# Optimization experiments

Measured on AMD Instinct MI355X. Metric: run time of the kernel, lower is better.

Reference implementation:

```python
import jax, jax.numpy as jnp
import numpy as np

HEADS = 8  # from init_kwargs

def setup_inputs() -> dict:
    key = jax.random.key(0)
    ks = jax.random.split(key, 9)
    N, S, E = 8, 2048, 512
    scale = 1.0 / np.sqrt(E)
    return {
        "values": jax.random.normal(ks[0], (N, S, E), jnp.float32),
        "keys": jax.random.normal(ks[1], (N, S, E), jnp.float32),
        "query": jax.random.normal(ks[2], (N, S, E), jnp.float32),
        "mask": jnp.ones((N, 1, 1, S), jnp.int32),
        "Wv": jax.random.normal(ks[3], (E, E), jnp.float32) * scale,
        "Wk": jax.random.normal(ks[4], (E, E), jnp.float32) * scale,
        "Wq": jax.random.normal(ks[5], (E, E), jnp.float32) * scale,
        "Wo": jax.random.normal(ks[6], (E, E), jnp.float32) * scale,
        "bo": jnp.zeros((E,), jnp.float32),
    }

def reference(values, keys, query, mask, Wv, Wk, Wq, Wo, bo):
    N, Q, E = query.shape
    H = HEADS
    D = E // H
    v = (values @ Wv).reshape(N, -1, H, D)  # [N,K,H,D]
    k = (keys @ Wk).reshape(N, -1, H, D)
    q = (query @ Wq).reshape(N, Q, H, D)
    energy = jnp.einsum('nqhd,nkhd->nhqk', q, k)  # [N,H,Q,K]
    energy = jnp.where(mask == 0, jnp.float32(-1e20), energy)
    attn = jax.nn.softmax(energy / jnp.sqrt(jnp.float32(D)), axis=3)
    out = jnp.einsum('nhqk,nkhd->nqhd', attn, v).reshape(N, Q, E)
    return out @ Wo + bo
```

## Files before the change

### kernel.cpp

```cpp
#include <hip/hip_runtime.h>
#include <hip/hip_bf16.h>
#include <stdint.h>

typedef __bf16 bf16;
typedef __bf16 bf16x8 __attribute__((ext_vector_type(8)));
typedef __bf16 bf16x4v __attribute__((ext_vector_type(4)));
typedef float  f32x4  __attribute__((ext_vector_type(4)));
typedef float  f32x16 __attribute__((ext_vector_type(16)));
typedef unsigned int u32x4 __attribute__((ext_vector_type(4)));

#define NB    8
#define SEQ   2048
#define EMB   512
#define NHEAD 8
#define HD    64

static __device__ __forceinline__ f32x4 mfma16(bf16x8 a, bf16x8 b, f32x4 c) {
    return __builtin_amdgcn_mfma_f32_16x16x32_bf16(a, b, c, 0, 0, 0);
}
static __device__ __forceinline__ f32x16 mfma32(bf16x8 a, bf16x8 b, f32x16 c) {
    return __builtin_amdgcn_mfma_f32_32x32x16_bf16(a, b, c, 0, 0, 0);
}
static __device__ __forceinline__ float ex2(float x) {
    float r; asm("v_exp_f32 %0, %1" : "=v"(r) : "v"(x)); return r;
}
static __device__ __forceinline__ unsigned pkbf(float lo, float hi) {
    unsigned d; asm("v_cvt_pk_bf16_f32 %0, %1, %2" : "=v"(d) : "v"(lo), "v"(hi)); return d;
}
static __device__ __forceinline__ void gload_lds16(const void* g, void* l) {
    __builtin_amdgcn_global_load_lds(
        (const __attribute__((address_space(1))) unsigned int*)g,
        (__attribute__((address_space(3))) unsigned int*)l, 16, 0, 0);
}

__global__ __launch_bounds__(256) void prep_weights(
    const float* __restrict__ Wv, const float* __restrict__ Wk,
    const float* __restrict__ Wq, const float* __restrict__ Wo,
    bf16* __restrict__ wt)
{
    int idx = blockIdx.x * 256 + threadIdx.x;
    int w   = idx >> 18;
    int rem = idx & 262143;
    int k   = rem >> 9;
    int n   = rem & 511;
    const float* src = (w == 0) ? Wv : (w == 1) ? Wk : (w == 2) ? Wq : Wo;
    wt[(size_t)w * 262144 + (size_t)n * 512 + k] = (bf16)src[k * 512 + n];
}

template <bool A_F32, bool FINAL>
__global__ __launch_bounds__(256) void gemm_kernel(
    const void* __restrict__ Ap, const bf16* __restrict__ Bt,
    void* __restrict__ Cp, const float* __restrict__ bias)
{
    __shared__ __align__(16) bf16 As[128][72];
    __shared__ __align__(16) bf16 Bs[128][72];

    const int t    = threadIdx.x;
    const int lane = t & 63;
    const int wave = t >> 6;
    const int wr   = wave >> 1, wc = wave & 1;
    const int l15  = lane & 15, lg = lane >> 4;
    const long row0 = (long)blockIdx.x * 128;
    const int  col0 = blockIdx.y * 128;

    f32x4 acc[4][4];
#pragma unroll
    for (int i = 0; i < 4; i++)
#pragma unroll
        for (int j = 0; j < 4; j++) acc[i][j] = (f32x4){0.f, 0.f, 0.f, 0.f};

    for (int k0 = 0; k0 < 512; k0 += 64) {
        __syncthreads();
        if (A_F32) {
            const float* A = (const float*)Ap;
#pragma unroll
            for (int i = 0; i < 8; i++) {
                int c  = t + 256 * i;
                int r  = c >> 4;
                int cc = (c & 15) * 4;
                f32x4 v = *(const f32x4*)(A + (row0 + r) * 512 + k0 + cc);
                bf16x4v pk = { (bf16)v[0], (bf16)v[1], (bf16)v[2], (bf16)v[3] };
                *(bf16x4v*)&As[r][cc] = pk;
            }
        } else {
            const bf16* A = (const bf16*)Ap;
#pragma unroll
            for (int i = 0; i < 4; i++) {
                int c  = t + 256 * i;
                int r  = c >> 3;
                int cc = (c & 7) * 8;
                *(bf16x8*)&As[r][cc] = *(const bf16x8*)(A + (row0 + r) * 512 + k0 + cc);
            }
        }
#pragma unroll
        for (int i = 0; i < 4; i++) {
            int c  = t + 256 * i;
            int r  = c >> 3;
            int cc = (c & 7) * 8;
            *(bf16x8*)&Bs[r][cc] = *(const bf16x8*)(Bt + (size_t)(col0 + r) * 512 + k0 + cc);
        }
        __syncthreads();
#pragma unroll
        for (int kc = 0; kc < 64; kc += 32) {
            bf16x8 af[4], bfv[4];
#pragma unroll
            for (int mb = 0; mb < 4; mb++)
                af[mb] = *(bf16x8*)&As[wr * 64 + mb * 16 + l15][kc + lg * 8];
#pragma unroll
            for (int nb = 0; nb < 4; nb++)
                bfv[nb] = *(bf16x8*)&Bs[wc * 64 + nb * 16 + l15][kc + lg * 8];
#pragma unroll
            for (int mb = 0; mb < 4; mb++)
#pragma unroll
                for (int nb = 0; nb < 4; nb++)
                    acc[mb][nb] = mfma16(af[mb], bfv[nb], acc[mb][nb]);
        }
    }

#pragma unroll
    for (int mb = 0; mb < 4; mb++)
#pragma unroll
        for (int nb = 0; nb < 4; nb++)
#pragma unroll
            for (int r = 0; r < 4; r++) {
                long grow = row0 + wr * 64 + mb * 16 + lg * 4 + r;
                int  gcol = col0 + wc * 64 + nb * 16 + l15;
                float v = acc[mb][nb][r];
                if (FINAL) {
                    ((float*)Cp)[grow * 512 + gcol] = v + bias[gcol];
                } else {
                    ((bf16*)Cp)[grow * 512 + gcol] = (bf16)v;
                }
            }
}

__global__ __launch_bounds__(512, 2) void attn_kernel(
    const bf16* __restrict__ Qg, const bf16* __restrict__ Kg,
    const bf16* __restrict__ Vg, const int* __restrict__ mask,
    bf16* __restrict__ ctx)
{
    __shared__ __align__(16) bf16 Ks[2][4096];
    __shared__ __align__(16) bf16 Vt[2][4096];
    __shared__ __align__(16) bf16 Ob[8][32 * 72];

    const int t    = threadIdx.x;
    const int lane = t & 63;
    const int w    = t >> 6;
    const int l31  = lane & 31;
    const int hi   = lane >> 5;
    const int qt = blockIdx.x, h = blockIdx.y, n = blockIdx.z;

    const size_t nbase   = (size_t)n * SEQ;
    const size_t headoff = (size_t)h * 64;
    const int q0 = qt * 512 + w * 64;

    bf16x8 qf[2][4];
#pragma unroll
    for (int qb = 0; qb < 2; ++qb)
#pragma unroll
        for (int ds = 0; ds < 4; ++ds)
            qf[qb][ds] = *(const bf16x8*)(Qg + (nbase + q0 + qb * 32 + l31) * 512 + headoff + ds * 16 + hi * 8);

    f32x16 o[2][2] = {};
    float m_run[2] = {-1e30f, -1e30f};
    float l_run[2] = {0.f, 0.f};

    const bf16* kg = Kg + (nbase + w * 8 + (lane >> 3)) * 512 + headoff + (((lane & 7) ^ (lane >> 3)) << 3);
    const bf16* vg = Vg + (nbase + lane) * 512 + headoff + w * 8;
    const int*  mp = mask + n * SEQ;

    gload_lds16(kg, (char*)&Ks[0][0] + w * 1024);
    {
        bf16x8 v0 = *(const bf16x8*)vg;
        char* vb = (char*)&Vt[0][0];
#pragma unroll
        for (int j = 0; j < 8; ++j)
            *(bf16*)(vb + (8 * w + j) * 128 + ((2 * lane) ^ (j << 4))) = v0[j];
    }
    __syncthreads();

    const float SC = 0.18033688011f;

    int cur = 0;
    for (int kt = 0; kt < 32; ++kt) {
        bf16x8 vstage;
        if (kt < 31) {
            gload_lds16(kg + (size_t)(kt + 1) * 64 * 512, (char*)&Ks[cur ^ 1][0] + w * 1024);
            vstage = *(const bf16x8*)(vg + (size_t)(kt + 1) * 64 * 512);
        }
        int mv = mp[kt * 64 + lane];

        f32x16 p[2][2] = {};
        const char* kb_base = (const char*)&Ks[cur][0];
#pragma unroll
        for (int ds = 0; ds < 4; ++ds) {
            int sw = (ds * 32 + hi * 16) ^ ((l31 & 7) << 4);
            bf16x8 kf0 = *(const bf16x8*)(kb_base + (l31) * 128 + sw);
            bf16x8 kf1 = *(const bf16x8*)(kb_base + (32 + l31) * 128 + sw);
            p[0][0] = mfma32(kf0, qf[0][ds], p[0][0]);
            p[1][0] = mfma32(kf0, qf[1][ds], p[1][0]);
            p[0][1] = mfma32(kf1, qf[0][ds], p[0][1]);
            p[1][1] = mfma32(kf1, qf[1][ds], p[1][1]);
        }

        unsigned long long mb = __ballot(mv != 0);
        if (mb != ~0ULL) {
#pragma unroll
            for (int qb = 0; qb < 2; ++qb)
#pragma unroll
                for (int kb = 0; kb < 2; ++kb) {
                    float* pp = (float*)&p[qb][kb];
#pragma unroll
                    for (int r = 0; r < 16; ++r) {
                        int kk = kb * 32 + (r & 3) + 8 * (r >> 2) + 4 * hi;
                        if (!((mb >> kk) & 1)) pp[r] = -1e30f;
                    }
                }
        }

        u32x4 bq[2][4];
#pragma unroll
        for (int qb = 0; qb < 2; ++qb) {
            float* p0 = (float*)&p[qb][0];
            float* p1 = (float*)&p[qb][1];
            float tm = fmaxf(p0[0], p1[0]);
#pragma unroll
            for (int r = 1; r < 16; ++r) tm = fmaxf(tm, fmaxf(p0[r], p1[r]));
            float tms = tm * SC;
            float rmax = fmaxf(tms, __shfl_xor(tms, 32));
            if (!__all(rmax <= m_run[qb] + 8.0f)) {
                float mn  = fmaxf(m_run[qb], rmax);
                float fac = ex2(m_run[qb] - mn);
#pragma unroll
                for (int db = 0; db < 2; ++db) {
                    float* oo = (float*)&o[db][qb];
#pragma unroll
                    for (int r = 0; r < 16; ++r) oo[r] *= fac;
                }
                l_run[qb] *= fac;
                m_run[qb] = mn;
            }
            float negm = -m_run[qb];
            float sl = 0.f;
#pragma unroll
            for (int r = 0; r < 16; ++r) { float e = ex2(fmaf(p0[r], SC, negm)); p0[r] = e; sl += e; }
#pragma unroll
            for (int r = 0; r < 16; ++r) { float e = ex2(fmaf(p1[r], SC, negm)); p1[r] = e; sl += e; }
            l_run[qb] += sl + __shfl_xor(sl, 32);

#pragma unroll
            for (int ks = 0; ks < 4; ++ks) {
                float* ps = (ks >> 1) ? p1 : p0;
                int bo = (ks & 1) * 8;
                unsigned A  = pkbf(ps[bo + 0], ps[bo + 1]);
                unsigned B  = pkbf(ps[bo + 2], ps[bo + 3]);
                unsigned C  = pkbf(ps[bo + 4], ps[bo + 5]);
                unsigned Dw = pkbf(ps[bo + 6], ps[bo + 7]);
                unsigned xA = __shfl_xor(A, 32);
                unsigned xB = __shfl_xor(B, 32);
                unsigned xC = __shfl_xor(C, 32);
                unsigned xD = __shfl_xor(Dw, 32);
                unsigned w0 = hi ? xC : A;
                unsigned w1 = hi ? xD : B;
                unsigned w2 = hi ? C : xA;
                unsigned w3 = hi ? Dw : xB;
                bq[qb][ks] = (u32x4){w0, w1, w2, w3};
            }
        }

        const char* vb_base = (const char*)&Vt[cur][0];
#pragma unroll
        for (int ks = 0; ks < 4; ++ks) {
            int sw = (ks * 32 + hi * 16) ^ ((l31 & 7) << 4);
            bf16x8 vf0 = *(const bf16x8*)(vb_base + (l31) * 128 + sw);
            bf16x8 vf1 = *(const bf16x8*)(vb_base + (32 + l31) * 128 + sw);
            union { u32x4 u; bf16x8 v; } c0, c1;
            c0.u = bq[0][ks]; c1.u = bq[1][ks];
            o[0][0] = mfma32(vf0, c0.v, o[0][0]);
            o[0][1] = mfma32(vf0, c1.v, o[0][1]);
            o[1][0] = mfma32(vf1, c0.v, o[1][0]);
            o[1][1] = mfma32(vf1, c1.v, o[1][1]);
        }

        if (kt < 31) {
            char* vb = (char*)&Vt[cur ^ 1][0];
#pragma unroll
            for (int j = 0; j < 8; ++j)
                *(bf16*)(vb + (8 * w + j) * 128 + ((2 * lane) ^ (j << 4))) = vstage[j];
        }
        __syncthreads();
        cur ^= 1;
    }

#pragma unroll
    for (int qb = 0; qb < 2; ++qb) {
        float inv = 1.f / l_run[qb];
        bf16* ob = &Ob[w][0];
#pragma unroll
        for (int db = 0; db < 2; ++db) {
            float* oo = (float*)&o[db][qb];
#pragma unroll
            for (int r = 0; r < 16; ++r) {
                int d = db * 32 + (r & 3) + 8 * (r >> 2) + 4 * hi;
                ob[l31 * 72 + d] = (bf16)(oo[r] * inv);
            }
        }
#pragma unroll
        for (int i = 0; i < 2; ++i)
#pragma unroll
            for (int half = 0; half < 2; ++half) {
                int ql = i * 16 + (lane >> 2);
                int d8 = (lane & 3) * 8 + half * 32;
                bf16x8 vv = *(const bf16x8*)(ob + ql * 72 + d8);
                *(bf16x8*)(ctx + (nbase + q0 + qb * 32 + ql) * 512 + headoff + d8) = vv;
            }
    }
}

extern "C" void kernel_launch(void* const* d_in, const int* in_sizes, int n_in,
                              void* d_out, int out_size, void* d_ws, size_t ws_size,
                              hipStream_t stream) {
    (void)in_sizes; (void)n_in; (void)out_size; (void)ws_size;
    const float* values = (const float*)d_in[0];
    const float* keys   = (const float*)d_in[1];
    const float* query  = (const float*)d_in[2];
    const int*   mask   = (const int*)d_in[3];
    const float* Wv = (const float*)d_in[4];
    const float* Wk = (const float*)d_in[5];
    const float* Wq = (const float*)d_in[6];
    const float* Wo = (const float*)d_in[7];
    const float* bo = (const float*)d_in[8];
    float* out = (float*)d_out;

    char* ws = (char*)d_ws;
    bf16* wt = (bf16*)(ws);
    bf16* Qb = (bf16*)(ws + ((size_t)2  << 20));
    bf16* Kb = (bf16*)(ws + ((size_t)18 << 20));
    bf16* Vb = (bf16*)(ws + ((size_t)34 << 20));
    bf16* Cb = (bf16*)(ws + ((size_t)50 << 20));

    prep_weights<<<4096, 256, 0, stream>>>(Wv, Wk, Wq, Wo, wt);
    gemm_kernel<true, false><<<dim3(128, 4), 256, 0, stream>>>(values, wt,              Vb, nullptr);
    gemm_kernel<true, false><<<dim3(128, 4), 256, 0, stream>>>(keys,   wt + 262144,     Kb, nullptr);
    gemm_kernel<true, false><<<dim3(128, 4), 256, 0, stream>>>(query,  wt + 2 * 262144, Qb, nullptr);
    attn_kernel<<<dim3(4, 8, 8), 512, 0, stream>>>(Qb, Kb, Vb, mask, Cb);
    gemm_kernel<false, true><<<dim3(128, 4), 256, 0, stream>>>(Cb, wt + 3 * 262144, out, bo);
}
```

Measured before the change: 183.6 us.

## Halve attention query tile per wave to double grid and occupancy

Each wave in the attention kernel now handles 32 query rows instead of 64, so a block covers 256 queries. The grid grows from 256 to 512 blocks and launch bounds allow 4 blocks per CU. The aim is better CU fill and latency hiding on a 256-CU part. In exchange, each K/V tile loaded into LDS is reused across half as many queries, so K/V global traffic and LDS loads per FLOP double.

Measured after the change: 205.1 us. 11.7% more time.

```diff
diff --git a/kernel.cpp b/kernel.cpp
--- a/kernel.cpp
+++ b/kernel.cpp
@@ -134,7 +134,7 @@
             }
 }
 
-__global__ __launch_bounds__(512, 2) void attn_kernel(
+__global__ __launch_bounds__(512, 4) void attn_kernel(
     const bf16* __restrict__ Qg, const bf16* __restrict__ Kg,
     const bf16* __restrict__ Vg, const int* __restrict__ mask,
     bf16* __restrict__ ctx)
@@ -152,18 +152,16 @@
 
     const size_t nbase   = (size_t)n * SEQ;
     const size_t headoff = (size_t)h * 64;
-    const int q0 = qt * 512 + w * 64;
-
-    bf16x8 qf[2][4];
-#pragma unroll
-    for (int qb = 0; qb < 2; ++qb)
-#pragma unroll
-        for (int ds = 0; ds < 4; ++ds)
-            qf[qb][ds] = *(const bf16x8*)(Qg + (nbase + q0 + qb * 32 + l31) * 512 + headoff + ds * 16 + hi * 8);
-
-    f32x16 o[2][2] = {};
-    float m_run[2] = {-1e30f, -1e30f};
-    float l_run[2] = {0.f, 0.f};
+    const int q0 = qt * 256 + w * 32;
+
+    bf16x8 qf[4];
+#pragma unroll
+    for (int ds = 0; ds < 4; ++ds)
+        qf[ds] = *(const bf16x8*)(Qg + (nbase + q0 + l31) * 512 + headoff + ds * 16 + hi * 8);
+
+    f32x16 o[2] = {};
+    float m_run = -1e30f;
+    float l_run = 0.f;
 
     const bf16* kg = Kg + (nbase + w * 8 + (lane >> 3)) * 512 + headoff + (((lane & 7) ^ (lane >> 3)) << 3);
     const bf16* vg = Vg + (nbase + lane) * 512 + headoff + w * 8;
@@ -190,63 +188,58 @@
         }
         int mv = mp[kt * 64 + lane];
 
-        f32x16 p[2][2] = {};
+        f32x16 p[2] = {};
         const char* kb_base = (const char*)&Ks[cur][0];
 #pragma unroll
         for (int ds = 0; ds < 4; ++ds) {
             int sw = (ds * 32 + hi * 16) ^ ((l31 & 7) << 4);
             bf16x8 kf0 = *(const bf16x8*)(kb_base + (l31) * 128 + sw);
             bf16x8 kf1 = *(const bf16x8*)(kb_base + (32 + l31) * 128 + sw);
-            p[0][0] = mfma32(kf0, qf[0][ds], p[0][0]);
-            p[1][0] = mfma32(kf0, qf[1][ds], p[1][0]);
-            p[0][1] = mfma32(kf1, qf[0][ds], p[0][1]);
-            p[1][1] = mfma32(kf1, qf[1][ds], p[1][1]);
+            p[0] = mfma32(kf0, qf[ds], p[0]);
+            p[1] = mfma32(kf1, qf[ds], p[1]);
         }
 
         unsigned long long mb = __ballot(mv != 0);
         if (mb != ~0ULL) {
 #pragma unroll
-            for (int qb = 0; qb < 2; ++qb)
-#pragma unroll
-                for (int kb = 0; kb < 2; ++kb) {
-                    float* pp = (float*)&p[qb][kb];
-#pragma unroll
-                    for (int r = 0; r < 16; ++r) {
-                        int kk = kb * 32 + (r & 3) + 8 * (r >> 2) + 4 * hi;
-                        if (!((mb >> kk) & 1)) pp[r] = -1e30f;
-                    }
+            for (int kb = 0; kb < 2; ++kb) {
+                float* pp = (float*)&p[kb];
+#pragma unroll
+                for (int r = 0; r < 16; ++r) {
+                    int kk = kb * 32 + (r & 3) + 8 * (r >> 2) + 4 * hi;
+                    if (!((mb >> kk) & 1)) pp[r] = -1e30f;
                 }
-        }
-
-        u32x4 bq[2][4];
-#pragma unroll
-        for (int qb = 0; qb < 2; ++qb) {
-            float* p0 = (float*)&p[qb][0];
-            float* p1 = (float*)&p[qb][1];
+            }
+        }
+
+        u32x4 bq[4];
+        {
+            float* p0 = (float*)&p[0];
+            float* p1 = (float*)&p[1];
             float tm = fmaxf(p0[0], p1[0]);
 #pragma unroll
             for (int r = 1; r < 16; ++r) tm = fmaxf(tm, fmaxf(p0[r], p1[r]));
             float tms = tm * SC;
             float rmax = fmaxf(tms, __shfl_xor(tms, 32));
-            if (!__all(rmax <= m_run[qb] + 8.0f)) {
-                float mn  = fmaxf(m_run[qb], rmax);
-                float fac = ex2(m_run[qb] - mn);
+            if (!__all(rmax <= m_run + 8.0f)) {
+                float mn  = fmaxf(m_run, rmax);
+                float fac = ex2(m_run - mn);
 #pragma unroll
                 for (int db = 0; db < 2; ++db) {
-                    float* oo = (float*)&o[db][qb];
+                    float* oo = (float*)&o[db];
 #pragma unroll
                     for (int r = 0; r < 16; ++r) oo[r] *= fac;
                 }
-                l_run[qb] *= fac;
-                m_run[qb] = mn;
-            }
-            float negm = -m_run[qb];
+                l_run *= fac;
+                m_run = mn;
+            }
+            float negm = -m_run;
             float sl = 0.f;
 #pragma unroll
             for (int r = 0; r < 16; ++r) { float e = ex2(fmaf(p0[r], SC, negm)); p0[r] = e; sl += e; }
 #pragma unroll
             for (int r = 0; r < 16; ++r) { float e = ex2(fmaf(p1[r], SC, negm)); p1[r] = e; sl += e; }
-            l_run[qb] += sl + __shfl_xor(sl, 32);
+            l_run += sl + __shfl_xor(sl, 32);
 
 #pragma unroll
             for (int ks = 0; ks < 4; ++ks) {
@@ -264,7 +257,7 @@
                 unsigned w1 = hi ? xD : B;
                 unsigned w2 = hi ? C : xA;
                 unsigned w3 = hi ? Dw : xB;
-                bq[qb][ks] = (u32x4){w0, w1, w2, w3};
+                bq[ks] = (u32x4){w0, w1, w2, w3};
             }
         }
 
@@ -274,12 +267,10 @@
             int sw = (ks * 32 + hi * 16) ^ ((l31 & 7) << 4);
             bf16x8 vf0 = *(const bf16x8*)(vb_base + (l31) * 128 + sw);
             bf16x8 vf1 = *(const bf16x8*)(vb_base + (32 + l31) * 128 + sw);
-            union { u32x4 u; bf16x8 v; } c0, c1;
-            c0.u = bq[0][ks]; c1.u = bq[1][ks];
-            o[0][0] = mfma32(vf0, c0.v, o[0][0]);
-            o[0][1] = mfma32(vf0, c1.v, o[0][1]);
-            o[1][0] = mfma32(vf1, c0.v, o[1][0]);
-            o[1][1] = mfma32(vf1, c1.v, o[1][1]);
+            union { u32x4 u; bf16x8 v; } c0;
+            c0.u = bq[ks];
+            o[0] = mfma32(vf0, c0.v, o[0]);
+            o[1] = mfma32(vf1, c0.v, o[1]);
         }
 
         if (kt < 31) {
@@ -292,13 +283,12 @@
         cur ^= 1;
     }
 
-#pragma unroll
-    for (int qb = 0; qb < 2; ++qb) {
-        float inv = 1.f / l_run[qb];
+    {
+        float inv = 1.f / l_run;
         bf16* ob = &Ob[w][0];
 #pragma unroll
         for (int db = 0; db < 2; ++db) {
-            float* oo = (float*)&o[db][qb];
+            float* oo = (float*)&o[db];
 #pragma unroll
             for (int r = 0; r < 16; ++r) {
                 int d = db * 32 + (r & 3) + 8 * (r >> 2) + 4 * hi;
@@ -312,7 +302,7 @@
                 int ql = i * 16 + (lane >> 2);
                 int d8 = (lane & 3) * 8 + half * 32;
                 bf16x8 vv = *(const bf16x8*)(ob + ql * 72 + d8);
-                *(bf16x8*)(ctx + (nbase + q0 + qb * 32 + ql) * 512 + headoff + d8) = vv;
+                *(bf16x8*)(ctx + (nbase + q0 + ql) * 512 + headoff + d8) = vv;
             }
     }
 }
@@ -343,6 +333,6 @@
     gemm_kernel<true, false><<<dim3(128, 4), 256, 0, stream>>>(values, wt,              Vb, nullptr);
     gemm_kernel<true, false><<<dim3(128, 4), 256, 0, stream>>>(keys,   wt + 262144,     Kb, nullptr);
     gemm_kernel<true, false><<<dim3(128, 4), 256, 0, stream>>>(query,  wt + 2 * 262144, Qb, nullptr);
-    attn_kernel<<<dim3(4, 8, 8), 512, 0, stream>>>(Qb, Kb, Vb, mask, Cb);
+    attn_kernel<<<dim3(8, 8, 8), 512, 0, stream>>>(Qb, Kb, Vb, mask, Cb);
     gemm_kernel<false, true><<<dim3(128, 4), 256, 0, stream>>>(Cb, wt + 3 * 262144, out, bo);
 }
```

## Process two key tiles per barrier and overlap QK of one with PV of the other

Applied to the files above, without the earlier changes.

The attention loop now handles two 64-key tiles per iteration. K and V buffers grow to four slots, so there is one barrier per pair of tiles and the next pair is prefetched ahead. Inside an iteration, the QK MFMAs of the second tile are issued next to the PV MFMAs of the first tile, and the MFMA blocks are wrapped in s_setprio. A block-wide precheck of the mask skips the per-tile mask loads and ballots when every mask entry is set. The row-max reduction now uses a max3 tree, and the exp-sum uses four separate accumulators. In exchange, LDS use per block and register pressure go up, since an extra bq copy must be kept live.

Result: faster. 179.8 us (-2.1%).

```diff
diff --git a/kernel.cpp b/kernel.cpp
--- a/kernel.cpp
+++ b/kernel.cpp
@@ -27,11 +27,16 @@
 static __device__ __forceinline__ unsigned pkbf(float lo, float hi) {
     unsigned d; asm("v_cvt_pk_bf16_f32 %0, %1, %2" : "=v"(d) : "v"(lo), "v"(hi)); return d;
 }
+static __device__ __forceinline__ float max3(float a, float b, float c) {
+    return fmaxf(fmaxf(a, b), c);
+}
 static __device__ __forceinline__ void gload_lds16(const void* g, void* l) {
     __builtin_amdgcn_global_load_lds(
         (const __attribute__((address_space(1))) unsigned int*)g,
         (__attribute__((address_space(3))) unsigned int*)l, 16, 0, 0);
 }
+#define PRIO1 __builtin_amdgcn_s_setprio(1)
+#define PRIO0 __builtin_amdgcn_s_setprio(0)
 
 __global__ __launch_bounds__(256) void prep_weights(
     const float* __restrict__ Wv, const float* __restrict__ Wk,
@@ -139,8 +144,8 @@
     const bf16* __restrict__ Vg, const int* __restrict__ mask,
     bf16* __restrict__ ctx)
 {
-    __shared__ __align__(16) bf16 Ks[2][4096];
-    __shared__ __align__(16) bf16 Vt[2][4096];
+    __shared__ __align__(16) bf16 Ks[4][4096];
+    __shared__ __align__(16) bf16 Vt[4][4096];
     __shared__ __align__(16) bf16 Ob[8][32 * 72];
 
     const int t    = threadIdx.x;
@@ -154,6 +159,14 @@
     const size_t headoff = (size_t)h * 64;
     const int q0 = qt * 512 + w * 64;
 
+    int* mflags = (int*)&Ob[0][0];
+    {
+        const int* mp0 = mask + n * SEQ + t * 4;
+        int mok = (mp0[0] != 0) & (mp0[1] != 0) & (mp0[2] != 0) & (mp0[3] != 0);
+        unsigned long long b = __ballot(mok);
+        if (lane == 0) mflags[w] = (b == ~0ULL) ? 1 : 0;
+    }
+
     bf16x8 qf[2][4];
 #pragma unroll
     for (int qb = 0; qb < 2; ++qb)
@@ -169,127 +182,175 @@
     const bf16* vg = Vg + (nbase + lane) * 512 + headoff + w * 8;
     const int*  mp = mask + n * SEQ;
 
-    gload_lds16(kg, (char*)&Ks[0][0] + w * 1024);
-    {
-        bf16x8 v0 = *(const bf16x8*)vg;
-        char* vb = (char*)&Vt[0][0];
-#pragma unroll
-        for (int j = 0; j < 8; ++j)
-            *(bf16*)(vb + (8 * w + j) * 128 + ((2 * lane) ^ (j << 4))) = v0[j];
-    }
+#define VSCAT(VR, VB) do {                                                    \
+        char* vbp = (char*)(VB);                                              \
+        _Pragma("unroll") for (int j = 0; j < 8; ++j)                         \
+            *(bf16*)(vbp + (8 * w + j) * 128 + ((2 * lane) ^ (j << 4))) = (VR)[j]; \
+    } while (0)
+
+    gload_lds16(kg,                     (char*)&Ks[0][0] + w * 1024);
+    gload_lds16(kg + (size_t)64 * 512,  (char*)&Ks[1][0] + w * 1024);
+    bf16x8 vrA = *(const bf16x8*)vg;
+    bf16x8 vrB = *(const bf16x8*)(vg + (size_t)64 * 512);
+    VSCAT(vrA, &Vt[0][0]);
+    VSCAT(vrB, &Vt[1][0]);
     __syncthreads();
+    const int maskall = mflags[0] & mflags[1] & mflags[2] & mflags[3] &
+                        mflags[4] & mflags[5] & mflags[6] & mflags[7];
 
     const float SC = 0.18033688011f;
 
-    int cur = 0;
-    for (int kt = 0; kt < 32; ++kt) {
-        bf16x8 vstage;
-        if (kt < 31) {
-            gload_lds16(kg + (size_t)(kt + 1) * 64 * 512, (char*)&Ks[cur ^ 1][0] + w * 1024);
-            vstage = *(const bf16x8*)(vg + (size_t)(kt + 1) * 64 * 512);
-        }
-        int mv = mp[kt * 64 + lane];
-
-        f32x16 p[2][2] = {};
-        const char* kb_base = (const char*)&Ks[cur][0];
-#pragma unroll
-        for (int ds = 0; ds < 4; ++ds) {
-            int sw = (ds * 32 + hi * 16) ^ ((l31 & 7) << 4);
-            bf16x8 kf0 = *(const bf16x8*)(kb_base + (l31) * 128 + sw);
-            bf16x8 kf1 = *(const bf16x8*)(kb_base + (32 + l31) * 128 + sw);
-            p[0][0] = mfma32(kf0, qf[0][ds], p[0][0]);
-            p[1][0] = mfma32(kf0, qf[1][ds], p[1][0]);
-            p[0][1] = mfma32(kf1, qf[0][ds], p[0][1]);
-            p[1][1] = mfma32(kf1, qf[1][ds], p[1][1]);
-        }
-
-        unsigned long long mb = __ballot(mv != 0);
-        if (mb != ~0ULL) {
-#pragma unroll
-            for (int qb = 0; qb < 2; ++qb)
-#pragma unroll
-                for (int kb = 0; kb < 2; ++kb) {
-                    float* pp = (float*)&p[qb][kb];
-#pragma unroll
-                    for (int r = 0; r < 16; ++r) {
-                        int kk = kb * 32 + (r & 3) + 8 * (r >> 2) + 4 * hi;
-                        if (!((mb >> kk) & 1)) pp[r] = -1e30f;
-                    }
-                }
-        }
-
-        u32x4 bq[2][4];
-#pragma unroll
-        for (int qb = 0; qb < 2; ++qb) {
-            float* p0 = (float*)&p[qb][0];
-            float* p1 = (float*)&p[qb][1];
-            float tm = fmaxf(p0[0], p1[0]);
-#pragma unroll
-            for (int r = 1; r < 16; ++r) tm = fmaxf(tm, fmaxf(p0[r], p1[r]));
-            float tms = tm * SC;
-            float rmax = fmaxf(tms, __shfl_xor(tms, 32));
-            if (!__all(rmax <= m_run[qb] + 8.0f)) {
-                float mn  = fmaxf(m_run[qb], rmax);
-                float fac = ex2(m_run[qb] - mn);
-#pragma unroll
-                for (int db = 0; db < 2; ++db) {
-                    float* oo = (float*)&o[db][qb];
-#pragma unroll
-                    for (int r = 0; r < 16; ++r) oo[r] *= fac;
-                }
-                l_run[qb] *= fac;
-                m_run[qb] = mn;
-            }
-            float negm = -m_run[qb];
-            float sl = 0.f;
-#pragma unroll
-            for (int r = 0; r < 16; ++r) { float e = ex2(fmaf(p0[r], SC, negm)); p0[r] = e; sl += e; }
-#pragma unroll
-            for (int r = 0; r < 16; ++r) { float e = ex2(fmaf(p1[r], SC, negm)); p1[r] = e; sl += e; }
-            l_run[qb] += sl + __shfl_xor(sl, 32);
-
-#pragma unroll
-            for (int ks = 0; ks < 4; ++ks) {
-                float* ps = (ks >> 1) ? p1 : p0;
-                int bo = (ks & 1) * 8;
-                unsigned A  = pkbf(ps[bo + 0], ps[bo + 1]);
-                unsigned B  = pkbf(ps[bo + 2], ps[bo + 3]);
-                unsigned C  = pkbf(ps[bo + 4], ps[bo + 5]);
-                unsigned Dw = pkbf(ps[bo + 6], ps[bo + 7]);
-                unsigned xA = __shfl_xor(A, 32);
-                unsigned xB = __shfl_xor(B, 32);
-                unsigned xC = __shfl_xor(C, 32);
-                unsigned xD = __shfl_xor(Dw, 32);
-                unsigned w0 = hi ? xC : A;
-                unsigned w1 = hi ? xD : B;
-                unsigned w2 = hi ? C : xA;
-                unsigned w3 = hi ? Dw : xB;
-                bq[qb][ks] = (u32x4){w0, w1, w2, w3};
-            }
-        }
-
-        const char* vb_base = (const char*)&Vt[cur][0];
-#pragma unroll
-        for (int ks = 0; ks < 4; ++ks) {
-            int sw = (ks * 32 + hi * 16) ^ ((l31 & 7) << 4);
-            bf16x8 vf0 = *(const bf16x8*)(vb_base + (l31) * 128 + sw);
-            bf16x8 vf1 = *(const bf16x8*)(vb_base + (32 + l31) * 128 + sw);
-            union { u32x4 u; bf16x8 v; } c0, c1;
-            c0.u = bq[0][ks]; c1.u = bq[1][ks];
-            o[0][0] = mfma32(vf0, c0.v, o[0][0]);
-            o[0][1] = mfma32(vf0, c1.v, o[0][1]);
-            o[1][0] = mfma32(vf1, c0.v, o[1][0]);
-            o[1][1] = mfma32(vf1, c1.v, o[1][1]);
-        }
-
-        if (kt < 31) {
-            char* vb = (char*)&Vt[cur ^ 1][0];
-#pragma unroll
-            for (int j = 0; j < 8; ++j)
-                *(bf16*)(vb + (8 * w + j) * 128 + ((2 * lane) ^ (j << 4))) = vstage[j];
+    f32x16 p[2][2];
+    u32x4  bq[2][4];
+
+#define QK_TILE(KB) do {                                                      \
+        const char* kbb = (const char*)(KB);                                  \
+        f32x16 zz = {};                                                       \
+        p[0][0] = zz; p[0][1] = zz; p[1][0] = zz; p[1][1] = zz;               \
+        PRIO1;                                                                \
+        _Pragma("unroll")                                                     \
+        for (int ds = 0; ds < 4; ++ds) {                                      \
+            int sw = (ds * 32 + hi * 16) ^ ((l31 & 7) << 4);                  \
+            bf16x8 kf0 = *(const bf16x8*)(kbb + l31 * 128 + sw);              \
+            bf16x8 kf1 = *(const bf16x8*)(kbb + (32 + l31) * 128 + sw);       \
+            p[0][0] = mfma32(kf0, qf[0][ds], p[0][0]);                        \
+            p[1][0] = mfma32(kf0, qf[1][ds], p[1][0]);                        \
+            p[0][1] = mfma32(kf1, qf[0][ds], p[0][1]);                        \
+            p[1][1] = mfma32(kf1, qf[1][ds], p[1][1]);                        \
+        }                                                                     \
+        PRIO0;                                                                \
+    } while (0)
+
+#define MASK_TILE(T) do {                                                     \
+        if (!maskall) {                                                       \
+            int mv = mp[(T) * 64 + lane];                                     \
+            unsigned long long mb = __ballot(mv != 0);                        \
+            if (mb != ~0ULL) {                                                \
+                _Pragma("unroll") for (int qb = 0; qb < 2; ++qb)              \
+                _Pragma("unroll") for (int kb = 0; kb < 2; ++kb) {            \
+                    float* pp = (float*)&p[qb][kb];                           \
+                    _Pragma("unroll") for (int r = 0; r < 16; ++r) {          \
+                        int kk = kb * 32 + (r & 3) + 8 * (r >> 2) + 4 * hi;   \
+                        if (!((mb >> kk) & 1)) pp[r] = -1e30f;                \
+                    }                                                         \
+                }                                                             \
+            }                                                                 \
+        }                                                                     \
+    } while (0)
+
+#define SM_PACK do {                                                          \
+        _Pragma("unroll")                                                     \
+        for (int qb = 0; qb < 2; ++qb) {                                      \
+            float* p0 = (float*)&p[qb][0];                                    \
+            float* p1 = (float*)&p[qb][1];                                    \
+            float g0 = max3(p0[0], p0[1], p0[2]);                             \
+            float g1 = max3(p0[3], p0[4], p0[5]);                             \
+            float g2 = max3(p0[6], p0[7], p0[8]);                             \
+            float g3 = max3(p0[9], p0[10], p0[11]);                           \
+            float g4 = max3(p0[12], p0[13], p0[14]);                          \
+            float g5 = max3(p0[15], p1[0], p1[1]);                            \
+            float g6 = max3(p1[2], p1[3], p1[4]);                             \
+            float g7 = max3(p1[5], p1[6], p1[7]);                             \
+            float g8 = max3(p1[8], p1[9], p1[10]);                            \
+            float g9 = max3(p1[11], p1[12], p1[13]);                          \
+            float g10 = fmaxf(p1[14], p1[15]);                                \
+            float t0 = max3(g0, g1, g2), t1 = max3(g3, g4, g5);               \
+            float t2 = max3(g6, g7, g8), t3 = max3(g9, g10, t0);              \
+            float tm = max3(t1, t2, t3);                                      \
+            float tms = tm * SC;                                              \
+            float rmax = fmaxf(tms, __shfl_xor(tms, 32));                     \
+            if (!__all(rmax <= m_run[qb] + 8.0f)) {                           \
+                float mn  = fmaxf(m_run[qb], rmax);                           \
+                float fac = ex2(m_run[qb] - mn);                              \
+                _Pragma("unroll") for (int db = 0; db < 2; ++db) {            \
+                    float* oo = (float*)&o[db][qb];                           \
+                    _Pragma("unroll") for (int r = 0; r < 16; ++r) oo[r] *= fac; \
+                }                                                             \
+                l_run[qb] *= fac; m_run[qb] = mn;                             \
+            }                                                                 \
+            float negm = -m_run[qb];                                          \
+            float sa0 = 0.f, sa1 = 0.f, sa2 = 0.f, sa3 = 0.f;                 \
+            _Pragma("unroll") for (int r = 0; r < 16; r += 4) {               \
+                float e0 = ex2(fmaf(p0[r],   SC, negm)); p0[r]   = e0; sa0 += e0; \
+                float e1 = ex2(fmaf(p0[r+1], SC, negm)); p0[r+1] = e1; sa1 += e1; \
+                float e2 = ex2(fmaf(p0[r+2], SC, negm)); p0[r+2] = e2; sa2 += e2; \
+                float e3 = ex2(fmaf(p0[r+3], SC, negm)); p0[r+3] = e3; sa3 += e3; \
+            }                                                                 \
+            _Pragma("unroll") for (int r = 0; r < 16; r += 4) {               \
+                float e0 = ex2(fmaf(p1[r],   SC, negm)); p1[r]   = e0; sa0 += e0; \
+                float e1 = ex2(fmaf(p1[r+1], SC, negm)); p1[r+1] = e1; sa1 += e1; \
+                float e2 = ex2(fmaf(p1[r+2], SC, negm)); p1[r+2] = e2; sa2 += e2; \
+                float e3 = ex2(fmaf(p1[r+3], SC, negm)); p1[r+3] = e3; sa3 += e3; \
+            }                                                                 \
+            float sl = (sa0 + sa1) + (sa2 + sa3);                             \
+            l_run[qb] += sl + __shfl_xor(sl, 32);                             \
+            _Pragma("unroll")                                                 \
+            for (int ks = 0; ks < 4; ++ks) {                                  \
+                float* ps = (ks >> 1) ? p1 : p0;                              \
+                int bo = (ks & 1) * 8;                                        \
+                unsigned A  = pkbf(ps[bo + 0], ps[bo + 1]);                   \
+                unsigned B  = pkbf(ps[bo + 2], ps[bo + 3]);                   \
+                unsigned C  = pkbf(ps[bo + 4], ps[bo + 5]);                   \
+                unsigned Dw = pkbf(ps[bo + 6], ps[bo + 7]);                   \
+                unsigned xA = __shfl_xor(A, 32), xB = __shfl_xor(B, 32);      \
+                unsigned xC = __shfl_xor(C, 32), xD = __shfl_xor(Dw, 32);     \
+                unsigned w0 = hi ? xC : A, w1 = hi ? xD : B;                  \
+                unsigned w2 = hi ? C : xA, w3 = hi ? Dw : xB;                 \
+                bq[qb][ks] = (u32x4){w0, w1, w2, w3};                         \
+            }                                                                 \
+        }                                                                     \
+    } while (0)
+
+#define PV_TILE(VB) do {                                                      \
+        const char* vbb = (const char*)(VB);                                  \
+        PRIO1;                                                                \
+        _Pragma("unroll")                                                     \
+        for (int ks = 0; ks < 4; ++ks) {                                      \
+            int sw = (ks * 32 + hi * 16) ^ ((l31 & 7) << 4);                  \
+            bf16x8 vf0 = *(const bf16x8*)(vbb + l31 * 128 + sw);              \
+            bf16x8 vf1 = *(const bf16x8*)(vbb + (32 + l31) * 128 + sw);       \
+            union { u32x4 u; bf16x8 v; } c0, c1;                              \
+            c0.u = bq[0][ks]; c1.u = bq[1][ks];                               \
+            o[0][0] = mfma32(vf0, c0.v, o[0][0]);                             \
+            o[0][1] = mfma32(vf0, c1.v, o[0][1]);                             \
+            o[1][0] = mfma32(vf1, c0.v, o[1][0]);                             \
+            o[1][1] = mfma32(vf1, c1.v, o[1][1]);                             \
+        }                                                                     \
+        PRIO0;                                                                \
+    } while (0)
+
+    u32x4 bqA[2][4];
+
+    for (int e = 0; e < 16; ++e) {
+        const int bA = (e & 1) * 2, bB = bA + 1;
+        const int nA = bA ^ 2,      nB = bB ^ 2;
+        if (e < 15) {
+            gload_lds16(kg + (size_t)(2 * e + 2) * 64 * 512, (char*)&Ks[nA][0] + w * 1024);
+            gload_lds16(kg + (size_t)(2 * e + 3) * 64 * 512, (char*)&Ks[nB][0] + w * 1024);
+            vrA = *(const bf16x8*)(vg + (size_t)(2 * e + 2) * 64 * 512);
+            vrB = *(const bf16x8*)(vg + (size_t)(2 * e + 3) * 64 * 512);
+        }
+        QK_TILE(&Ks[bA][0]);
+        MASK_TILE(2 * e);
+        SM_PACK;
+#pragma unroll
+        for (int qb = 0; qb < 2; ++qb)
+#pragma unroll
+            for (int ks = 0; ks < 4; ++ks) bqA[qb][ks] = bq[qb][ks];
+        QK_TILE(&Ks[bB][0]);
+        PV_TILE(&Vt[bA][0]);
+#pragma unroll
+        for (int qb = 0; qb < 2; ++qb)
+#pragma unroll
+            for (int ks = 0; ks < 4; ++ks) bq[qb][ks] = bqA[qb][ks];
+        MASK_TILE(2 * e + 1);
+        SM_PACK;
+        PV_TILE(&Vt[bB][0]);
+        if (e < 15) {
+            VSCAT(vrA, &Vt[nA][0]);
+            VSCAT(vrB, &Vt[nB][0]);
         }
         __syncthreads();
-        cur ^= 1;
     }
 
 #pragma unroll
@@ -315,6 +376,11 @@
                 *(bf16x8*)(ctx + (nbase + q0 + qb * 32 + ql) * 512 + headoff + d8) = vv;
             }
     }
+#undef VSCAT
+#undef QK_TILE
+#undef MASK_TILE
+#undef SM_PACK
+#undef PV_TILE
 }
 
 extern "C" void kernel_launch(void* const* d_in, const int* in_sizes, int n_in,
```
